# Kernel optimization log

Measured on AMD Instinct MI355X. Metric: run time of the kernel, lower is better.

The kernel has to match this reference:

```python
import jax, jax.numpy as jnp
import numpy as np
from numpy.lib.stride_tricks import sliding_window_view

# Static configuration matching init_kwargs
F_, H_, W_ = 2, 32, 32          # video_shape
K = 5                            # kernel_size (odd)
HEADS, DIM_HEAD = 8, 64
N = F_ * H_ * W_                 # number of video tokens (2048)
PAD = K // 2
INNER = HEADS * DIM_HEAD         # 512


def _neighbors():
    # Flattened token index at each (f,h,w); pad with sentinel N (out of bounds -> zeros / masked)
    idx = np.arange(N, dtype=np.int32).reshape(F_, H_, W_)
    padded = np.full((F_ + 2 * PAD, H_ + 2 * PAD, W_ + 2 * PAD), N, dtype=np.int32)
    padded[PAD:PAD + F_, PAD:PAD + H_, PAD:PAD + W_] = idx
    # sliding_window_view matches unfoldNd's kernel-offset ordering (kf, kh, kw row-major)
    return sliding_window_view(padded, (K, K, K)).reshape(N, K ** 3)


NBR = jnp.asarray(_neighbors())                                   # [N, K^3]
# causal: query i attends only to neighbors with index <= i; prepend BOS column (never masked)
CAUSAL = jnp.pad(jnp.arange(N)[:, None] < NBR, ((0, 0), (1, 0)))  # [N, K^3 + 1]


def setup_inputs() -> dict:
    key = jax.random.key(0)
    k1, k2, k3 = jax.random.split(key, 3)
    return {
        "x": jax.random.normal(k1, (1, N, INNER), jnp.float32),
        "w_qkv": jax.random.normal(k2, (INNER, 3 * INNER), jnp.float32) * 0.02,
        "w_out": jax.random.normal(k3, (INNER, INNER), jnp.float32) * 0.02,
        "b_out": jnp.zeros((INNER,), jnp.float32),
    }


def reference(x, w_qkv, w_out, b_out):
    b, n, dim = x.shape            # n == N
    bh = b * HEADS
    scale = DIM_HEAD ** -0.5

    xp = jnp.pad(x, ((0, 0), (0, 1), (0, 0)))        # pad one zero token at the end: [b, n+1, dim]
    qkv = xp @ w_qkv                                  # [b, n+1, 3*inner]
    q, kk, vv = jnp.split(qkv, 3, axis=-1)

    def split_heads(t):  # 'b n (h d) -> (b h) n d'
        return t.reshape(b, n + 1, HEADS, DIM_HEAD).transpose(0, 2, 1, 3).reshape(bh, n + 1, DIM_HEAD)

    q, kk, vv = map(split_heads, (q, kk, vv))
    q = q[:, 1:] * scale                              # drop BOS query: [bh, n, d]
    k_bos, kk = kk[:, :1], kk[:, 1:]                  # BOS kv + n spatial tokens
    v_bos, vv = vv[:, :1], vv[:, 1:]

    # Append a zero row so the sentinel index N gathers zeros (== unfold's zero padding)
    zero = jnp.zeros((bh, 1, DIM_HEAD), kk.dtype)
    kw = jnp.concatenate([kk, zero], axis=1)[:, NBR]  # [bh, n, K^3, d]
    vw = jnp.concatenate([vv, zero], axis=1)[:, NBR]

    bos_k = jnp.broadcast_to(k_bos[:, None], (bh, n, 1, DIM_HEAD))
    bos_v = jnp.broadcast_to(v_bos[:, None], (bh, n, 1, DIM_HEAD))
    kw = jnp.concatenate([bos_k, kw], axis=2)         # [bh, n, K^3+1, d]
    vw = jnp.concatenate([bos_v, vw], axis=2)

    sim = jnp.einsum('bid,bijd->bij', q, kw)          # [bh, n, K^3+1]
    sim = jnp.where(CAUSAL[:n], -jnp.finfo(sim.dtype).max, sim)
    attn = jax.nn.softmax(sim, axis=-1)
    out = jnp.einsum('bij,bijd->bid', attn, vw)       # [bh, n, d]

    out = jnp.concatenate([v_bos, out], axis=1)       # BOS output = its value: [bh, n+1, d]
    out = out.reshape(b, HEADS, n + 1, DIM_HEAD).transpose(0, 2, 1, 3).reshape(b, n + 1, INNER)
    return (out @ w_out + b_out)[:, :n]
```

## Files before the change

kernel.cpp:

```cpp
#include <hip/hip_runtime.h>
#include <hip/hip_bf16.h>

#define NTOK  2048
#define INNER 512
#define KDIM  512
#define QKVP  1536

typedef __attribute__((ext_vector_type(8))) short bf16x8;
typedef __attribute__((ext_vector_type(4))) float f32x4;

__device__ __forceinline__ unsigned short f2b(float f) {
  unsigned int u = __float_as_uint(f);
  return (unsigned short)((u + 0x7FFFu + ((u >> 16) & 1u)) >> 16);
}

__device__ __forceinline__ void async_copy16(const unsigned short* g, unsigned short* l) {
  __builtin_amdgcn_global_load_lds((const __attribute__((address_space(1))) void*)g,
                                   (__attribute__((address_space(3))) void*)l, 16, 0, 0);
}

__global__ __launch_bounds__(256) void prep(const float* __restrict__ w_qkv,
                                            const float* __restrict__ w_out,
                                            const float* __restrict__ x,
                                            unsigned short* __restrict__ wqkvT,
                                            unsigned short* __restrict__ woutT,
                                            unsigned short* __restrict__ xb,
                                            int* __restrict__ glist,
                                            int* __restrict__ gcnt) {
  __shared__ float tile[32][33];
  __shared__ int list[192];
  __shared__ int cntS;
  const int tid = threadIdx.x;
  int b = blockIdx.x;

  if (b >= 1152) {
    const int i = (b - 1152) * 1024 + tid * 4;
    float4 v = *(const float4*)(x + i);
    ushort4 o;
    o.x = f2b(v.x); o.y = f2b(v.y); o.z = f2b(v.z); o.w = f2b(v.w);
    *(ushort4*)(xb + i) = o;
    return;
  }

  if (b < 1024) {
    const float* in; unsigned short* out; int K, N, bx, by;
    if (b < 768) { in = w_qkv; out = wqkvT; K = 512; N = 1536; bx = b % 48; by = b / 48; }
    else { int bb = b - 768; in = w_out; out = woutT; K = 512; N = 512; bx = bb & 15; by = bb >> 4; }
    const int k0 = by * 32, n0 = bx * 32;
    const int r = tid >> 3, c4 = (tid & 7) * 4;
    float4 v = *(const float4*)(in + (size_t)(k0 + r) * N + n0 + c4);
    tile[r][c4 + 0] = v.x; tile[r][c4 + 1] = v.y;
    tile[r][c4 + 2] = v.z; tile[r][c4 + 3] = v.w;
    __syncthreads();
    ushort4 o;
    o.x = f2b(tile[c4 + 0][r]);
    o.y = f2b(tile[c4 + 1][r]);
    o.z = f2b(tile[c4 + 2][r]);
    o.w = f2b(tile[c4 + 3][r]);
    *(ushort4*)(out + (size_t)(n0 + r) * K + k0 + c4) = o;
    return;
  }

  const int pt = b - 1024;
  const int f  = pt >> 6;
  const int hh = (pt >> 1) & 31;
  const int w0 = (pt & 1) << 4;

  if (tid < 192) list[tid] = 0x7FFFFFFF;
  if (tid == 0) { list[0] = 0; cntS = 1; }
  __syncthreads();
  if (tid >= 1 && tid <= 160) {
    int cc = tid - 1;
    int p = cc / 20, wo = cc - p * 20;
    int ff = (p < 5) ? 0 : 1;
    int h2 = hh - 2 + ((p < 5) ? p : (p - 5));
    bool ok = (p < 5) ? ((f == 1) ? (h2 >= 0 && h2 <= 31) : (p <= 2 && h2 >= 0))
                      : (f == 1 && h2 >= 0);
    if (ok) {
      bool diag = (ff == f) && (h2 == hh);
      int wlo = max(0, w0 - 2);
      int whi = min(31, diag ? (w0 + 15) : (w0 + 17));
      int w2 = wlo + wo;
      if (w2 <= whi) {
        int pos = atomicAdd(&cntS, 1);
        list[pos] = ((ff << 10) | (h2 << 5) | w2) + 1;
      }
    }
  }
  __syncthreads();
  if (tid < 192) glist[pt * 192 + tid] = list[tid];
  if (tid == 0) gcnt[pt] = cntS;
}

__global__ __launch_bounds__(256, 4) void gemm_qkv(const unsigned short* __restrict__ A,
                                                   const unsigned short* __restrict__ Bt,
                                                   unsigned short* __restrict__ C) {
  constexpr int BK = 32, N = 1536, K = 512;
  __shared__ __align__(16) unsigned short As[64 * BK];
  __shared__ __align__(16) unsigned short Bs[64 * BK];
  const int tid = threadIdx.x, lane = tid & 63, wave = tid >> 6;
  const int m0 = blockIdx.y * 64, n0 = blockIdx.x * 64;
  const int wm = (wave >> 1) * 32, wn = (wave & 1) * 32;
  const int li = tid * 8, r = li >> 5, c = li & 31;
  const int fr = lane & 15, fk = (lane >> 4) * 8;

  f32x4 acc[2][2] = {};

  for (int k0 = 0; k0 < K; k0 += BK) {
    async_copy16(A  + (size_t)(m0 + r) * K + k0 + c, &As[li]);
    async_copy16(Bt + (size_t)(n0 + r) * K + k0 + c, &Bs[li]);
    __syncthreads();
    bf16x8 af[2], bfr[2];
#pragma unroll
    for (int i = 0; i < 2; ++i) af[i] = *(const bf16x8*)&As[(wm + i * 16 + fr) * BK + fk];
#pragma unroll
    for (int j = 0; j < 2; ++j) bfr[j] = *(const bf16x8*)&Bs[(wn + j * 16 + fr) * BK + fk];
#pragma unroll
    for (int i = 0; i < 2; ++i)
#pragma unroll
      for (int j = 0; j < 2; ++j)
        acc[i][j] = __builtin_amdgcn_mfma_f32_16x16x32_bf16(af[i], bfr[j], acc[i][j], 0, 0, 0);
    __syncthreads();
  }

  const int er = (lane >> 4) * 4, ec = lane & 15;
#pragma unroll
  for (int i = 0; i < 2; ++i)
#pragma unroll
    for (int j = 0; j < 2; ++j) {
      const int col = n0 + wn + j * 16 + ec;
#pragma unroll
      for (int rr = 0; rr < 4; ++rr) {
        const int row = m0 + wm + i * 16 + er + rr;
        C[(size_t)row * N + col] = f2b(acc[i][j][rr]);
      }
    }
}

__global__ __launch_bounds__(256, 4) void gemm_out(const unsigned short* __restrict__ A,
                                                   const unsigned short* __restrict__ Bt,
                                                   const float* __restrict__ bias,
                                                   float* __restrict__ C) {
  constexpr int BK = 32, N = 512, K = 512;
  __shared__ __align__(16) unsigned short As[32 * BK];
  __shared__ __align__(16) unsigned short Bs[64 * BK];
  const int tid = threadIdx.x, lane = tid & 63, wave = tid >> 6;
  const int m0 = blockIdx.y * 32, n0 = blockIdx.x * 64;
  const int wm = (wave >> 1) * 16, wn = (wave & 1) * 32;
  const int li = tid * 8, r = li >> 5, c = li & 31;
  const int fr = lane & 15, fk = (lane >> 4) * 8;

  f32x4 acc[2] = {};

  for (int k0 = 0; k0 < K; k0 += BK) {
    if (tid < 128) async_copy16(A + (size_t)(m0 + r) * K + k0 + c, &As[li]);
    async_copy16(Bt + (size_t)(n0 + r) * K + k0 + c, &Bs[li]);
    __syncthreads();
    bf16x8 af, bfr[2];
    af = *(const bf16x8*)&As[(wm + fr) * BK + fk];
#pragma unroll
    for (int j = 0; j < 2; ++j) bfr[j] = *(const bf16x8*)&Bs[(wn + j * 16 + fr) * BK + fk];
#pragma unroll
    for (int j = 0; j < 2; ++j)
      acc[j] = __builtin_amdgcn_mfma_f32_16x16x32_bf16(af, bfr[j], acc[j], 0, 0, 0);
    __syncthreads();
  }

  const int er = (lane >> 4) * 4, ec = lane & 15;
#pragma unroll
  for (int j = 0; j < 2; ++j) {
    const int col = n0 + wn + j * 16 + ec;
    const float b = bias[col];
#pragma unroll
    for (int rr = 0; rr < 4; ++rr) {
      const int row = m0 + wm + er + rr;
      C[(size_t)row * N + col] = acc[j][rr] + b;
    }
  }
}

__global__ __launch_bounds__(256) void attn_mfma(const unsigned short* __restrict__ qkv,
                                                 const int* __restrict__ glist,
                                                 const int* __restrict__ gcnt,
                                                 unsigned short* __restrict__ O) {
  __shared__ __align__(16) int list[192];
  __shared__ __align__(16) float mOd[2][16][72];
  __shared__ float mM[2][16], mL[2][16];
  __shared__ int cntS;

  const int tid = threadIdx.x;
  const int hp = blockIdx.y;

  if (blockIdx.x == 128) {
    if (tid < 128) O[hp * 128 + tid] = qkv[1024 + hp * 128 + tid];
    return;
  }
  const int pt = blockIdx.x;
  const int f  = pt >> 6;
  const int hh = (pt >> 1) & 31;
  const int w0 = (pt & 1) << 4;
  const int base_i = (f << 10) | (hh << 5) | w0;

  if (tid < 192) list[tid] = glist[pt * 192 + tid];
  if (tid == 0) cntS = gcnt[pt];
  __syncthreads();
  const int nsub = (cntS + 15) >> 4;

  const int lane = tid & 63;
  const int wave = tid >> 6;
  const int hw   = wave >> 1;
  const int half = wave & 1;
  const int head = hp * 2 + hw;
  const int quad = lane >> 4;
  const int ec   = lane & 15;

  const int i_q = base_i + ec;
  const int tq  = min(i_q + 1, 2047);
  const unsigned short* qrow = qkv + (size_t)tq * QKVP + head * 64 + quad * 8;
  const bf16x8 qb0 = *(const bf16x8*)(qrow);
  const bf16x8 qb1 = *(const bf16x8*)(qrow + 32);

  f32x4 Od[4] = {{0,0,0,0},{0,0,0,0},{0,0,0,0},{0,0,0,0}};
  float m = -1e30f, l = 0.0f;

  for (int sub = half; sub < nsub; sub += 2) {
    const int base = sub * 16;
    const int tok_e = list[base + ec];
    const int4 tokv = *(const int4*)&list[base + quad * 4];
    const int tk[4] = {tokv.x, tokv.y, tokv.z, tokv.w};

    f32x4 S = {0, 0, 0, 0};
    {
      const int t0 = (tok_e > 2047) ? 0 : tok_e;
      const unsigned short* kr = qkv + (size_t)t0 * QKVP + 512 + head * 64 + quad * 8;
      const bf16x8 kf0 = *(const bf16x8*)(kr);
      const bf16x8 kf1 = *(const bf16x8*)(kr + 32);
      S = __builtin_amdgcn_mfma_f32_16x16x32_bf16(kf0, qb0, S, 0, 0, 0);
      S = __builtin_amdgcn_mfma_f32_16x16x32_bf16(kf1, qb1, S, 0, 0, 0);
    }

    float Sm[4];
#pragma unroll
    for (int r = 0; r < 4; ++r) {
      const int tok = tk[r];
      const int idx = tok - 1;
      const bool v = (tok == 0) ||
                     ((idx <= i_q) && ((unsigned)((idx & 31) - (w0 + ec) + 2) <= 4u));
      Sm[r] = v ? S[r] * 0.125f : -1e30f;
    }
    float mx = fmaxf(fmaxf(Sm[0], Sm[1]), fmaxf(Sm[2], Sm[3]));
    mx = fmaxf(mx, __shfl_xor(mx, 16, 64));
    mx = fmaxf(mx, __shfl_xor(mx, 32, 64));
    const float mn = fmaxf(m, mx);
    const float corr = __expf(m - mn);
    m = mn;
    const float p0 = __expf(Sm[0] - mn);
    const float p1 = __expf(Sm[1] - mn);
    const float p2 = __expf(Sm[2] - mn);
    const float p3 = __expf(Sm[3] - mn);
    float rs = (p0 + p1) + (p2 + p3);
    rs += __shfl_xor(rs, 16, 64);
    rs += __shfl_xor(rs, 32, 64);
    l = l * corr + rs;

    bf16x8 pf;
    pf[0] = (short)f2b(p0); pf[1] = (short)f2b(p1);
    pf[2] = (short)f2b(p2); pf[3] = (short)f2b(p3);
    pf[4] = 0; pf[5] = 0; pf[6] = 0; pf[7] = 0;

    const unsigned short* vp[4];
#pragma unroll
    for (int j = 0; j < 4; ++j) {
      const int tv = (tk[j] > 2047) ? 0 : tk[j];
      vp[j] = qkv + (size_t)tv * QKVP + 1024 + head * 64 + ec;
    }
#pragma unroll
    for (int dt = 0; dt < 4; ++dt) {
      bf16x8 vf;
#pragma unroll
      for (int j = 0; j < 4; ++j) vf[j] = (short)vp[j][dt * 16];
      vf[4] = 0; vf[5] = 0; vf[6] = 0; vf[7] = 0;
#pragma unroll
      for (int r = 0; r < 4; ++r) Od[dt][r] *= corr;
      Od[dt] = __builtin_amdgcn_mfma_f32_16x16x32_bf16(vf, pf, Od[dt], 0, 0, 0);
    }
  }

  if (half == 1) {
#pragma unroll
    for (int dt = 0; dt < 4; ++dt)
      *(f32x4*)&mOd[hw][ec][dt * 16 + quad * 4] = Od[dt];
    if (quad == 0) { mM[hw][ec] = m; mL[hw][ec] = l; }
  }
  __syncthreads();
  if (half == 0 && i_q <= 2046) {
    const float m1 = mM[hw][ec], l1 = mL[hw][ec];
    const float mm = fmaxf(m, m1);
    const float c0 = __expf(m - mm), c1 = __expf(m1 - mm);
    const float rl = 1.0f / (l * c0 + l1 * c1);
    unsigned short* ob = O + (size_t)(i_q + 1) * 512 + head * 64 + quad * 4;
#pragma unroll
    for (int dt = 0; dt < 4; ++dt) {
      const f32x4 o1 = *(const f32x4*)&mOd[hw][ec][dt * 16 + quad * 4];
      ushort4 u;
      u.x = f2b((Od[dt][0] * c0 + o1[0] * c1) * rl);
      u.y = f2b((Od[dt][1] * c0 + o1[1] * c1) * rl);
      u.z = f2b((Od[dt][2] * c0 + o1[2] * c1) * rl);
      u.w = f2b((Od[dt][3] * c0 + o1[3] * c1) * rl);
      *(ushort4*)(ob + dt * 16) = u;
    }
  }
}


extern "C" void kernel_launch(void* const* d_in, const int* in_sizes, int n_in,
                              void* d_out, int out_size, void* d_ws, size_t ws_size,
                              hipStream_t stream) {
  const float* x     = (const float*)d_in[0];
  const float* w_qkv = (const float*)d_in[1];
  const float* w_out = (const float*)d_in[2];
  const float* b_out = (const float*)d_in[3];
  float* out = (float*)d_out;

  char* ws = (char*)d_ws;
  unsigned short* qkvb  = (unsigned short*)(ws);
  unsigned short* wqkvT = (unsigned short*)(ws + 6291456);
  unsigned short* woutT = (unsigned short*)(ws + 7864320);
  unsigned short* Ob    = (unsigned short*)(ws + 8388608);
  unsigned short* xb    = (unsigned short*)(ws + 10485760);
  int*            glist = (int*)(ws + 12582912);
  int*            gcnt  = (int*)(ws + 12681216);

  hipLaunchKernelGGL(prep, dim3(2176), dim3(256), 0, stream,
                     w_qkv, w_out, x, wqkvT, woutT, xb, glist, gcnt);

  hipLaunchKernelGGL(gemm_qkv, dim3(24, 32), dim3(256), 0, stream, xb, wqkvT, qkvb);

  hipLaunchKernelGGL(attn_mfma, dim3(129, 4), dim3(256), 0, stream, qkvb, glist, gcnt, Ob);

  hipLaunchKernelGGL(gemm_out, dim3(8, 64), dim3(256), 0, stream, Ob, woutT, b_out, out);
}
```

Before: 96.29 us.

## Fuse all four stages into one cooperative persistent kernel with grid syncs

Merges the prep, QKV GEMM, local attention and output GEMM kernels into a single cooperative kernel of 512 persistent blocks. Each stage loops over its original block indices with a grid stride and is separated from the next by grid.sync(). This removes three kernel launches and the gaps between them. In exchange it adds grid-wide barrier cost, loses the occupancy hint of launch bounds (256, 4) on the GEMMs, and makes each block's register and LDS budget the maximum needed by any stage.

```diff
diff --git a/kernel.cpp b/kernel.cpp
--- a/kernel.cpp
+++ b/kernel.cpp
@@ -1,5 +1,8 @@
 #include <hip/hip_runtime.h>
 #include <hip/hip_bf16.h>
+#include <hip/hip_cooperative_groups.h>
+
+namespace cg = cooperative_groups;
 
 #define NTOK  2048
 #define INNER 512
@@ -19,295 +22,302 @@
                                    (__attribute__((address_space(3))) void*)l, 16, 0, 0);
 }
 
-__global__ __launch_bounds__(256) void prep(const float* __restrict__ w_qkv,
+__global__ __launch_bounds__(256) void mega(const float* __restrict__ x,
+                                            const float* __restrict__ w_qkv,
                                             const float* __restrict__ w_out,
-                                            const float* __restrict__ x,
+                                            const float* __restrict__ b_out,
+                                            float* __restrict__ out,
+                                            unsigned short* __restrict__ qkvb,
                                             unsigned short* __restrict__ wqkvT,
                                             unsigned short* __restrict__ woutT,
+                                            unsigned short* __restrict__ Ob,
                                             unsigned short* __restrict__ xb,
                                             int* __restrict__ glist,
                                             int* __restrict__ gcnt) {
-  __shared__ float tile[32][33];
-  __shared__ int list[192];
-  __shared__ int cntS;
+  cg::grid_group grid = cg::this_grid();
+  __shared__ __align__(16) char smem[12544];
   const int tid = threadIdx.x;
-  int b = blockIdx.x;
-
-  if (b >= 1152) {
-    const int i = (b - 1152) * 1024 + tid * 4;
-    float4 v = *(const float4*)(x + i);
-    ushort4 o;
-    o.x = f2b(v.x); o.y = f2b(v.y); o.z = f2b(v.z); o.w = f2b(v.w);
-    *(ushort4*)(xb + i) = o;
-    return;
-  }
-
-  if (b < 1024) {
-    const float* in; unsigned short* out; int K, N, bx, by;
-    if (b < 768) { in = w_qkv; out = wqkvT; K = 512; N = 1536; bx = b % 48; by = b / 48; }
-    else { int bb = b - 768; in = w_out; out = woutT; K = 512; N = 512; bx = bb & 15; by = bb >> 4; }
-    const int k0 = by * 32, n0 = bx * 32;
-    const int r = tid >> 3, c4 = (tid & 7) * 4;
-    float4 v = *(const float4*)(in + (size_t)(k0 + r) * N + n0 + c4);
-    tile[r][c4 + 0] = v.x; tile[r][c4 + 1] = v.y;
-    tile[r][c4 + 2] = v.z; tile[r][c4 + 3] = v.w;
-    __syncthreads();
-    ushort4 o;
-    o.x = f2b(tile[c4 + 0][r]);
-    o.y = f2b(tile[c4 + 1][r]);
-    o.z = f2b(tile[c4 + 2][r]);
-    o.w = f2b(tile[c4 + 3][r]);
-    *(ushort4*)(out + (size_t)(n0 + r) * K + k0 + c4) = o;
-    return;
-  }
-
-  const int pt = b - 1024;
-  const int f  = pt >> 6;
-  const int hh = (pt >> 1) & 31;
-  const int w0 = (pt & 1) << 4;
-
-  if (tid < 192) list[tid] = 0x7FFFFFFF;
-  if (tid == 0) { list[0] = 0; cntS = 1; }
-  __syncthreads();
-  if (tid >= 1 && tid <= 160) {
-    int cc = tid - 1;
-    int p = cc / 20, wo = cc - p * 20;
-    int ff = (p < 5) ? 0 : 1;
-    int h2 = hh - 2 + ((p < 5) ? p : (p - 5));
-    bool ok = (p < 5) ? ((f == 1) ? (h2 >= 0 && h2 <= 31) : (p <= 2 && h2 >= 0))
-                      : (f == 1 && h2 >= 0);
-    if (ok) {
-      bool diag = (ff == f) && (h2 == hh);
-      int wlo = max(0, w0 - 2);
-      int whi = min(31, diag ? (w0 + 15) : (w0 + 17));
-      int w2 = wlo + wo;
-      if (w2 <= whi) {
-        int pos = atomicAdd(&cntS, 1);
-        list[pos] = ((ff << 10) | (h2 << 5) | w2) + 1;
-      }
+  const int nb  = gridDim.x;
+
+  {
+    float (*tile)[33] = (float(*)[33])smem;
+    int* list = (int*)(smem + 4224);
+    int* cntS = (int*)(smem + 4224 + 768);
+
+    for (int b = blockIdx.x; b < 2176; b += nb) {
+      if (b >= 1152) {
+        const int i = (b - 1152) * 1024 + tid * 4;
+        float4 v = *(const float4*)(x + i);
+        ushort4 o;
+        o.x = f2b(v.x); o.y = f2b(v.y); o.z = f2b(v.z); o.w = f2b(v.w);
+        *(ushort4*)(xb + i) = o;
+        continue;
+      }
+      if (b < 1024) {
+        const float* in; unsigned short* outw; int K, N, bx, by;
+        if (b < 768) { in = w_qkv; outw = wqkvT; K = 512; N = 1536; bx = b % 48; by = b / 48; }
+        else { int bb = b - 768; in = w_out; outw = woutT; K = 512; N = 512; bx = bb & 15; by = bb >> 4; }
+        const int k0 = by * 32, n0 = bx * 32;
+        const int r = tid >> 3, c4 = (tid & 7) * 4;
+        float4 v = *(const float4*)(in + (size_t)(k0 + r) * N + n0 + c4);
+        tile[r][c4 + 0] = v.x; tile[r][c4 + 1] = v.y;
+        tile[r][c4 + 2] = v.z; tile[r][c4 + 3] = v.w;
+        __syncthreads();
+        ushort4 o;
+        o.x = f2b(tile[c4 + 0][r]);
+        o.y = f2b(tile[c4 + 1][r]);
+        o.z = f2b(tile[c4 + 2][r]);
+        o.w = f2b(tile[c4 + 3][r]);
+        *(ushort4*)(outw + (size_t)(n0 + r) * K + k0 + c4) = o;
+        __syncthreads();
+        continue;
+      }
+      const int pt = b - 1024;
+      const int f  = pt >> 6;
+      const int hh = (pt >> 1) & 31;
+      const int w0 = (pt & 1) << 4;
+      if (tid < 192) list[tid] = 0x7FFFFFFF;
+      if (tid == 0) { list[0] = 0; *cntS = 1; }
+      __syncthreads();
+      if (tid >= 1 && tid <= 160) {
+        int cc = tid - 1;
+        int p = cc / 20, wo = cc - p * 20;
+        int ff = (p < 5) ? 0 : 1;
+        int h2 = hh - 2 + ((p < 5) ? p : (p - 5));
+        bool ok = (p < 5) ? ((f == 1) ? (h2 >= 0 && h2 <= 31) : (p <= 2 && h2 >= 0))
+                          : (f == 1 && h2 >= 0);
+        if (ok) {
+          bool diag = (ff == f) && (h2 == hh);
+          int wlo = max(0, w0 - 2);
+          int whi = min(31, diag ? (w0 + 15) : (w0 + 17));
+          int w2 = wlo + wo;
+          if (w2 <= whi) {
+            int pos = atomicAdd(cntS, 1);
+            list[pos] = ((ff << 10) | (h2 << 5) | w2) + 1;
+          }
+        }
+      }
+      __syncthreads();
+      if (tid < 192) glist[pt * 192 + tid] = list[tid];
+      if (tid == 0) gcnt[pt] = *cntS;
+      __syncthreads();
     }
   }
-  __syncthreads();
-  if (tid < 192) glist[pt * 192 + tid] = list[tid];
-  if (tid == 0) gcnt[pt] = cntS;
-}
-
-__global__ __launch_bounds__(256, 4) void gemm_qkv(const unsigned short* __restrict__ A,
-                                                   const unsigned short* __restrict__ Bt,
-                                                   unsigned short* __restrict__ C) {
-  constexpr int BK = 32, N = 1536, K = 512;
-  __shared__ __align__(16) unsigned short As[64 * BK];
-  __shared__ __align__(16) unsigned short Bs[64 * BK];
-  const int tid = threadIdx.x, lane = tid & 63, wave = tid >> 6;
-  const int m0 = blockIdx.y * 64, n0 = blockIdx.x * 64;
-  const int wm = (wave >> 1) * 32, wn = (wave & 1) * 32;
-  const int li = tid * 8, r = li >> 5, c = li & 31;
-  const int fr = lane & 15, fk = (lane >> 4) * 8;
-
-  f32x4 acc[2][2] = {};
-
-  for (int k0 = 0; k0 < K; k0 += BK) {
-    async_copy16(A  + (size_t)(m0 + r) * K + k0 + c, &As[li]);
-    async_copy16(Bt + (size_t)(n0 + r) * K + k0 + c, &Bs[li]);
-    __syncthreads();
-    bf16x8 af[2], bfr[2];
-#pragma unroll
-    for (int i = 0; i < 2; ++i) af[i] = *(const bf16x8*)&As[(wm + i * 16 + fr) * BK + fk];
-#pragma unroll
-    for (int j = 0; j < 2; ++j) bfr[j] = *(const bf16x8*)&Bs[(wn + j * 16 + fr) * BK + fk];
-#pragma unroll
-    for (int i = 0; i < 2; ++i)
-#pragma unroll
-      for (int j = 0; j < 2; ++j)
-        acc[i][j] = __builtin_amdgcn_mfma_f32_16x16x32_bf16(af[i], bfr[j], acc[i][j], 0, 0, 0);
-    __syncthreads();
-  }
-
-  const int er = (lane >> 4) * 4, ec = lane & 15;
-#pragma unroll
-  for (int i = 0; i < 2; ++i)
-#pragma unroll
-    for (int j = 0; j < 2; ++j) {
-      const int col = n0 + wn + j * 16 + ec;
-#pragma unroll
-      for (int rr = 0; rr < 4; ++rr) {
-        const int row = m0 + wm + i * 16 + er + rr;
-        C[(size_t)row * N + col] = f2b(acc[i][j][rr]);
-      }
-    }
-}
-
-__global__ __launch_bounds__(256, 4) void gemm_out(const unsigned short* __restrict__ A,
-                                                   const unsigned short* __restrict__ Bt,
-                                                   const float* __restrict__ bias,
-                                                   float* __restrict__ C) {
-  constexpr int BK = 32, N = 512, K = 512;
-  __shared__ __align__(16) unsigned short As[32 * BK];
-  __shared__ __align__(16) unsigned short Bs[64 * BK];
-  const int tid = threadIdx.x, lane = tid & 63, wave = tid >> 6;
-  const int m0 = blockIdx.y * 32, n0 = blockIdx.x * 64;
-  const int wm = (wave >> 1) * 16, wn = (wave & 1) * 32;
-  const int li = tid * 8, r = li >> 5, c = li & 31;
-  const int fr = lane & 15, fk = (lane >> 4) * 8;
-
-  f32x4 acc[2] = {};
-
-  for (int k0 = 0; k0 < K; k0 += BK) {
-    if (tid < 128) async_copy16(A + (size_t)(m0 + r) * K + k0 + c, &As[li]);
-    async_copy16(Bt + (size_t)(n0 + r) * K + k0 + c, &Bs[li]);
-    __syncthreads();
-    bf16x8 af, bfr[2];
-    af = *(const bf16x8*)&As[(wm + fr) * BK + fk];
-#pragma unroll
-    for (int j = 0; j < 2; ++j) bfr[j] = *(const bf16x8*)&Bs[(wn + j * 16 + fr) * BK + fk];
-#pragma unroll
-    for (int j = 0; j < 2; ++j)
-      acc[j] = __builtin_amdgcn_mfma_f32_16x16x32_bf16(af, bfr[j], acc[j], 0, 0, 0);
-    __syncthreads();
-  }
-
-  const int er = (lane >> 4) * 4, ec = lane & 15;
-#pragma unroll
-  for (int j = 0; j < 2; ++j) {
-    const int col = n0 + wn + j * 16 + ec;
-    const float b = bias[col];
-#pragma unroll
-    for (int rr = 0; rr < 4; ++rr) {
-      const int row = m0 + wm + er + rr;
-      C[(size_t)row * N + col] = acc[j][rr] + b;
+  grid.sync();
+
+  {
+    constexpr int BK = 32, N = 1536, K = 512;
+    unsigned short* As = (unsigned short*)smem;
+    unsigned short* Bs = (unsigned short*)(smem + 4096);
+    const int lane = tid & 63, wave = tid >> 6;
+    const int wm = (wave >> 1) * 32, wn = (wave & 1) * 32;
+    const int li = tid * 8, r = li >> 5, c = li & 31;
+    const int fr = lane & 15, fk = (lane >> 4) * 8;
+
+    for (int b = blockIdx.x; b < 768; b += nb) {
+      const int m0 = (b / 24) * 64, n0 = (b % 24) * 64;
+      f32x4 acc[2][2] = {};
+      for (int k0 = 0; k0 < K; k0 += BK) {
+        async_copy16(xb    + (size_t)(m0 + r) * K + k0 + c, &As[li]);
+        async_copy16(wqkvT + (size_t)(n0 + r) * K + k0 + c, &Bs[li]);
+        __syncthreads();
+        bf16x8 af[2], bfr[2];
+#pragma unroll
+        for (int i = 0; i < 2; ++i) af[i] = *(const bf16x8*)&As[(wm + i * 16 + fr) * BK + fk];
+#pragma unroll
+        for (int j = 0; j < 2; ++j) bfr[j] = *(const bf16x8*)&Bs[(wn + j * 16 + fr) * BK + fk];
+#pragma unroll
+        for (int i = 0; i < 2; ++i)
+#pragma unroll
+          for (int j = 0; j < 2; ++j)
+            acc[i][j] = __builtin_amdgcn_mfma_f32_16x16x32_bf16(af[i], bfr[j], acc[i][j], 0, 0, 0);
+        __syncthreads();
+      }
+      const int er = (lane >> 4) * 4, ec = lane & 15;
+#pragma unroll
+      for (int i = 0; i < 2; ++i)
+#pragma unroll
+        for (int j = 0; j < 2; ++j) {
+          const int col = n0 + wn + j * 16 + ec;
+#pragma unroll
+          for (int rr = 0; rr < 4; ++rr) {
+            const int row = m0 + wm + i * 16 + er + rr;
+            qkvb[(size_t)row * N + col] = f2b(acc[i][j][rr]);
+          }
+        }
     }
   }
-}
-
-__global__ __launch_bounds__(256) void attn_mfma(const unsigned short* __restrict__ qkv,
-                                                 const int* __restrict__ glist,
-                                                 const int* __restrict__ gcnt,
-                                                 unsigned short* __restrict__ O) {
-  __shared__ __align__(16) int list[192];
-  __shared__ __align__(16) float mOd[2][16][72];
-  __shared__ float mM[2][16], mL[2][16];
-  __shared__ int cntS;
-
-  const int tid = threadIdx.x;
-  const int hp = blockIdx.y;
-
-  if (blockIdx.x == 128) {
-    if (tid < 128) O[hp * 128 + tid] = qkv[1024 + hp * 128 + tid];
-    return;
-  }
-  const int pt = blockIdx.x;
-  const int f  = pt >> 6;
-  const int hh = (pt >> 1) & 31;
-  const int w0 = (pt & 1) << 4;
-  const int base_i = (f << 10) | (hh << 5) | w0;
-
-  if (tid < 192) list[tid] = glist[pt * 192 + tid];
-  if (tid == 0) cntS = gcnt[pt];
-  __syncthreads();
-  const int nsub = (cntS + 15) >> 4;
-
-  const int lane = tid & 63;
-  const int wave = tid >> 6;
-  const int hw   = wave >> 1;
-  const int half = wave & 1;
-  const int head = hp * 2 + hw;
-  const int quad = lane >> 4;
-  const int ec   = lane & 15;
-
-  const int i_q = base_i + ec;
-  const int tq  = min(i_q + 1, 2047);
-  const unsigned short* qrow = qkv + (size_t)tq * QKVP + head * 64 + quad * 8;
-  const bf16x8 qb0 = *(const bf16x8*)(qrow);
-  const bf16x8 qb1 = *(const bf16x8*)(qrow + 32);
-
-  f32x4 Od[4] = {{0,0,0,0},{0,0,0,0},{0,0,0,0},{0,0,0,0}};
-  float m = -1e30f, l = 0.0f;
-
-  for (int sub = half; sub < nsub; sub += 2) {
-    const int base = sub * 16;
-    const int tok_e = list[base + ec];
-    const int4 tokv = *(const int4*)&list[base + quad * 4];
-    const int tk[4] = {tokv.x, tokv.y, tokv.z, tokv.w};
-
-    f32x4 S = {0, 0, 0, 0};
-    {
-      const int t0 = (tok_e > 2047) ? 0 : tok_e;
-      const unsigned short* kr = qkv + (size_t)t0 * QKVP + 512 + head * 64 + quad * 8;
-      const bf16x8 kf0 = *(const bf16x8*)(kr);
-      const bf16x8 kf1 = *(const bf16x8*)(kr + 32);
-      S = __builtin_amdgcn_mfma_f32_16x16x32_bf16(kf0, qb0, S, 0, 0, 0);
-      S = __builtin_amdgcn_mfma_f32_16x16x32_bf16(kf1, qb1, S, 0, 0, 0);
-    }
-
-    float Sm[4];
-#pragma unroll
-    for (int r = 0; r < 4; ++r) {
-      const int tok = tk[r];
-      const int idx = tok - 1;
-      const bool v = (tok == 0) ||
-                     ((idx <= i_q) && ((unsigned)((idx & 31) - (w0 + ec) + 2) <= 4u));
-      Sm[r] = v ? S[r] * 0.125f : -1e30f;
-    }
-    float mx = fmaxf(fmaxf(Sm[0], Sm[1]), fmaxf(Sm[2], Sm[3]));
-    mx = fmaxf(mx, __shfl_xor(mx, 16, 64));
-    mx = fmaxf(mx, __shfl_xor(mx, 32, 64));
-    const float mn = fmaxf(m, mx);
-    const float corr = __expf(m - mn);
-    m = mn;
-    const float p0 = __expf(Sm[0] - mn);
-    const float p1 = __expf(Sm[1] - mn);
-    const float p2 = __expf(Sm[2] - mn);
-    const float p3 = __expf(Sm[3] - mn);
-    float rs = (p0 + p1) + (p2 + p3);
-    rs += __shfl_xor(rs, 16, 64);
-    rs += __shfl_xor(rs, 32, 64);
-    l = l * corr + rs;
-
-    bf16x8 pf;
-    pf[0] = (short)f2b(p0); pf[1] = (short)f2b(p1);
-    pf[2] = (short)f2b(p2); pf[3] = (short)f2b(p3);
-    pf[4] = 0; pf[5] = 0; pf[6] = 0; pf[7] = 0;
-
-    const unsigned short* vp[4];
-#pragma unroll
-    for (int j = 0; j < 4; ++j) {
-      const int tv = (tk[j] > 2047) ? 0 : tk[j];
-      vp[j] = qkv + (size_t)tv * QKVP + 1024 + head * 64 + ec;
-    }
-#pragma unroll
-    for (int dt = 0; dt < 4; ++dt) {
-      bf16x8 vf;
-#pragma unroll
-      for (int j = 0; j < 4; ++j) vf[j] = (short)vp[j][dt * 16];
-      vf[4] = 0; vf[5] = 0; vf[6] = 0; vf[7] = 0;
-#pragma unroll
-      for (int r = 0; r < 4; ++r) Od[dt][r] *= corr;
-      Od[dt] = __builtin_amdgcn_mfma_f32_16x16x32_bf16(vf, pf, Od[dt], 0, 0, 0);
+  grid.sync();
+
+  {
+    int* list   = (int*)smem;
+    float* mOd  = (float*)(smem + 768);
+    float* mM   = (float*)(smem + 9984);
+    float* mL   = (float*)(smem + 10112);
+    int* cntS   = (int*)(smem + 10240);
+
+    for (int b = blockIdx.x; b < 516; b += nb) {
+      const int pt = b >> 2;
+      const int hp = b & 3;
+      if (pt == 128) {
+        if (tid < 128) Ob[hp * 128 + tid] = qkvb[1024 + hp * 128 + tid];
+        continue;
+      }
+      const int f  = pt >> 6;
+      const int hh = (pt >> 1) & 31;
+      const int w0 = (pt & 1) << 4;
+      const int base_i = (f << 10) | (hh << 5) | w0;
+
+      if (tid < 192) list[tid] = glist[pt * 192 + tid];
+      if (tid == 0) *cntS = gcnt[pt];
+      __syncthreads();
+      const int nsub = (*cntS + 15) >> 4;
+
+      const int lane = tid & 63;
+      const int wave = tid >> 6;
+      const int hw   = wave >> 1;
+      const int half = wave & 1;
+      const int head = hp * 2 + hw;
+      const int quad = lane >> 4;
+      const int ec   = lane & 15;
+
+      const int i_q = base_i + ec;
+      const int tq  = min(i_q + 1, 2047);
+      const unsigned short* qrow = qkvb + (size_t)tq * QKVP + head * 64 + quad * 8;
+      const bf16x8 qb0 = *(const bf16x8*)(qrow);
+      const bf16x8 qb1 = *(const bf16x8*)(qrow + 32);
+
+      f32x4 Od[4] = {{0,0,0,0},{0,0,0,0},{0,0,0,0},{0,0,0,0}};
+      float m = -1e30f, l = 0.0f;
+
+      for (int sub = half; sub < nsub; sub += 2) {
+        const int base = sub * 16;
+        const int tok_e = list[base + ec];
+        const int4 tokv = *(const int4*)&list[base + quad * 4];
+        const int tk[4] = {tokv.x, tokv.y, tokv.z, tokv.w};
+
+        f32x4 S = {0, 0, 0, 0};
+        {
+          const int t0 = (tok_e > 2047) ? 0 : tok_e;
+          const unsigned short* kr = qkvb + (size_t)t0 * QKVP + 512 + head * 64 + quad * 8;
+          const bf16x8 kf0 = *(const bf16x8*)(kr);
+          const bf16x8 kf1 = *(const bf16x8*)(kr + 32);
+          S = __builtin_amdgcn_mfma_f32_16x16x32_bf16(kf0, qb0, S, 0, 0, 0);
+          S = __builtin_amdgcn_mfma_f32_16x16x32_bf16(kf1, qb1, S, 0, 0, 0);
+        }
+
+        float Sm[4];
+#pragma unroll
+        for (int r = 0; r < 4; ++r) {
+          const int tok = tk[r];
+          const int idx = tok - 1;
+          const bool v = (tok == 0) ||
+                         ((idx <= i_q) && ((unsigned)((idx & 31) - (w0 + ec) + 2) <= 4u));
+          Sm[r] = v ? S[r] * 0.125f : -1e30f;
+        }
+        float mx = fmaxf(fmaxf(Sm[0], Sm[1]), fmaxf(Sm[2], Sm[3]));
+        mx = fmaxf(mx, __shfl_xor(mx, 16, 64));
+        mx = fmaxf(mx, __shfl_xor(mx, 32, 64));
+        const float mn = fmaxf(m, mx);
+        const float corr = __expf(m - mn);
+        m = mn;
+        const float p0 = __expf(Sm[0] - mn);
+        const float p1 = __expf(Sm[1] - mn);
+        const float p2 = __expf(Sm[2] - mn);
+        const float p3 = __expf(Sm[3] - mn);
+        float rs = (p0 + p1) + (p2 + p3);
+        rs += __shfl_xor(rs, 16, 64);
+        rs += __shfl_xor(rs, 32, 64);
+        l = l * corr + rs;
+
+        bf16x8 pf;
+        pf[0] = (short)f2b(p0); pf[1] = (short)f2b(p1);
+        pf[2] = (short)f2b(p2); pf[3] = (short)f2b(p3);
+        pf[4] = 0; pf[5] = 0; pf[6] = 0; pf[7] = 0;
+
+        const unsigned short* vp[4];
+#pragma unroll
+        for (int j = 0; j < 4; ++j) {
+          const int tv = (tk[j] > 2047) ? 0 : tk[j];
+          vp[j] = qkvb + (size_t)tv * QKVP + 1024 + head * 64 + ec;
+        }
+#pragma unroll
+        for (int dt = 0; dt < 4; ++dt) {
+          bf16x8 vf;
+#pragma unroll
+          for (int j = 0; j < 4; ++j) vf[j] = (short)vp[j][dt * 16];
+          vf[4] = 0; vf[5] = 0; vf[6] = 0; vf[7] = 0;
+#pragma unroll
+          for (int r = 0; r < 4; ++r) Od[dt][r] *= corr;
+          Od[dt] = __builtin_amdgcn_mfma_f32_16x16x32_bf16(vf, pf, Od[dt], 0, 0, 0);
+        }
+      }
+
+      if (half == 1) {
+#pragma unroll
+        for (int dt = 0; dt < 4; ++dt)
+          *(f32x4*)&mOd[(hw * 16 + ec) * 72 + dt * 16 + quad * 4] = Od[dt];
+        if (quad == 0) { mM[hw * 16 + ec] = m; mL[hw * 16 + ec] = l; }
+      }
+      __syncthreads();
+      if (half == 0 && i_q <= 2046) {
+        const float m1 = mM[hw * 16 + ec], l1 = mL[hw * 16 + ec];
+        const float mm = fmaxf(m, m1);
+        const float c0 = __expf(m - mm), c1 = __expf(m1 - mm);
+        const float rl = 1.0f / (l * c0 + l1 * c1);
+        unsigned short* ob = Ob + (size_t)(i_q + 1) * 512 + head * 64 + quad * 4;
+#pragma unroll
+        for (int dt = 0; dt < 4; ++dt) {
+          const f32x4 o1 = *(const f32x4*)&mOd[(hw * 16 + ec) * 72 + dt * 16 + quad * 4];
+          ushort4 u;
+          u.x = f2b((Od[dt][0] * c0 + o1[0] * c1) * rl);
+          u.y = f2b((Od[dt][1] * c0 + o1[1] * c1) * rl);
+          u.z = f2b((Od[dt][2] * c0 + o1[2] * c1) * rl);
+          u.w = f2b((Od[dt][3] * c0 + o1[3] * c1) * rl);
+          *(ushort4*)(ob + dt * 16) = u;
+        }
+      }
+      __syncthreads();
     }
   }
-
-  if (half == 1) {
-#pragma unroll
-    for (int dt = 0; dt < 4; ++dt)
-      *(f32x4*)&mOd[hw][ec][dt * 16 + quad * 4] = Od[dt];
-    if (quad == 0) { mM[hw][ec] = m; mL[hw][ec] = l; }
-  }
-  __syncthreads();
-  if (half == 0 && i_q <= 2046) {
-    const float m1 = mM[hw][ec], l1 = mL[hw][ec];
-    const float mm = fmaxf(m, m1);
-    const float c0 = __expf(m - mm), c1 = __expf(m1 - mm);
-    const float rl = 1.0f / (l * c0 + l1 * c1);
-    unsigned short* ob = O + (size_t)(i_q + 1) * 512 + head * 64 + quad * 4;
-#pragma unroll
-    for (int dt = 0; dt < 4; ++dt) {
-      const f32x4 o1 = *(const f32x4*)&mOd[hw][ec][dt * 16 + quad * 4];
-      ushort4 u;
-      u.x = f2b((Od[dt][0] * c0 + o1[0] * c1) * rl);
-      u.y = f2b((Od[dt][1] * c0 + o1[1] * c1) * rl);
-      u.z = f2b((Od[dt][2] * c0 + o1[2] * c1) * rl);
-      u.w = f2b((Od[dt][3] * c0 + o1[3] * c1) * rl);
-      *(ushort4*)(ob + dt * 16) = u;
+  grid.sync();
+
+  {
+    constexpr int BK = 32, N = 512, K = 512;
+    unsigned short* As = (unsigned short*)smem;
+    unsigned short* Bs = (unsigned short*)(smem + 2048);
+    const int lane = tid & 63, wave = tid >> 6;
+    const int wm = (wave >> 1) * 16, wn = (wave & 1) * 32;
+    const int li = tid * 8, r = li >> 5, c = li & 31;
+    const int fr = lane & 15, fk = (lane >> 4) * 8;
+
+    for (int b = blockIdx.x; b < 512; b += nb) {
+      const int m0 = (b >> 3) * 32, n0 = (b & 7) * 64;
+      f32x4 acc[2] = {};
+      for (int k0 = 0; k0 < K; k0 += BK) {
+        if (tid < 128) async_copy16(Ob + (size_t)(m0 + r) * K + k0 + c, &As[li]);
+        async_copy16(woutT + (size_t)(n0 + r) * K + k0 + c, &Bs[li]);
+        __syncthreads();
+        bf16x8 af, bfr[2];
+        af = *(const bf16x8*)&As[(wm + fr) * BK + fk];
+#pragma unroll
+        for (int j = 0; j < 2; ++j) bfr[j] = *(const bf16x8*)&Bs[(wn + j * 16 + fr) * BK + fk];
+#pragma unroll
+        for (int j = 0; j < 2; ++j)
+          acc[j] = __builtin_amdgcn_mfma_f32_16x16x32_bf16(af, bfr[j], acc[j], 0, 0, 0);
+        __syncthreads();
+      }
+      const int er = (lane >> 4) * 4, ec = lane & 15;
+#pragma unroll
+      for (int j = 0; j < 2; ++j) {
+        const int col = n0 + wn + j * 16 + ec;
+        const float bb = b_out[col];
+#pragma unroll
+        for (int rr = 0; rr < 4; ++rr) {
+          const int row = m0 + wm + er + rr;
+          out[(size_t)row * N + col] = acc[j][rr] + bb;
+        }
+      }
     }
   }
 }
@@ -331,12 +341,8 @@
   int*            glist = (int*)(ws + 12582912);
   int*            gcnt  = (int*)(ws + 12681216);
 
-  hipLaunchKernelGGL(prep, dim3(2176), dim3(256), 0, stream,
-                     w_qkv, w_out, x, wqkvT, woutT, xb, glist, gcnt);
-
-  hipLaunchKernelGGL(gemm_qkv, dim3(24, 32), dim3(256), 0, stream, xb, wqkvT, qkvb);
-
-  hipLaunchKernelGGL(attn_mfma, dim3(129, 4), dim3(256), 0, stream, qkvb, glist, gcnt, Ob);
-
-  hipLaunchKernelGGL(gemm_out, dim3(8, 64), dim3(256), 0, stream, Ob, woutT, b_out, out);
+  void* kargs[] = {(void*)&x, (void*)&w_qkv, (void*)&w_out, (void*)&b_out, (void*)&out,
+                   (void*)&qkvb, (void*)&wqkvT, (void*)&woutT, (void*)&Ob, (void*)&xb,
+                   (void*)&glist, (void*)&gcnt};
+  hipLaunchCooperativeKernel((void*)mega, dim3(512), dim3(256), kargs, 0, stream);
 }
```

New measurement: 295.6 us. +207.0%, slower.

## Fuse fp32-to-bf16 conversion and neighbor list build into consumer kernels

Applied to the files above, without the earlier changes.

Removes the separate prep kernel. The QKV and output GEMMs now read fp32 x and weights directly, converting to bf16 while staging into LDS, and the attention kernel builds its causal neighbor list in shared memory instead of reading it from global memory. This cuts one launch and the round trips through the bf16 and list buffers. In exchange, the weight loads become strided scalar column reads, and the same weight conversion is repeated across every M-tile block rather than done once.

```diff
diff --git a/kernel.cpp b/kernel.cpp
--- a/kernel.cpp
+++ b/kernel.cpp
@@ -19,52 +19,88 @@
                                    (__attribute__((address_space(3))) void*)l, 16, 0, 0);
 }
 
-__global__ __launch_bounds__(256) void prep(const float* __restrict__ w_qkv,
-                                            const float* __restrict__ w_out,
-                                            const float* __restrict__ x,
-                                            unsigned short* __restrict__ wqkvT,
-                                            unsigned short* __restrict__ woutT,
-                                            unsigned short* __restrict__ xb,
-                                            int* __restrict__ glist,
-                                            int* __restrict__ gcnt) {
-  __shared__ float tile[32][33];
-  __shared__ int list[192];
+__global__ __launch_bounds__(256, 3) void gemm_qkv_f(const float* __restrict__ x,
+                                                     const float* __restrict__ w_qkv,
+                                                     unsigned short* __restrict__ C) {
+  constexpr int BK = 32, N = 1536, K = 512;
+  __shared__ __align__(16) unsigned short As[64 * BK];
+  __shared__ __align__(16) unsigned short Bs[64 * BK];
+  const int tid = threadIdx.x, lane = tid & 63, wave = tid >> 6;
+  const int m0 = blockIdx.y * 64, n0 = blockIdx.x * 64;
+  const int wm = (wave >> 1) * 32, wn = (wave & 1) * 32;
+  const int ar = tid >> 2, ac = (tid & 3) * 8;
+  const int bn = tid >> 2, bk8 = (tid & 3) * 8;
+  const int fr = lane & 15, fk = (lane >> 4) * 8;
+
+  f32x4 acc[2][2] = {};
+
+  for (int k0 = 0; k0 < K; k0 += BK) {
+    {
+      const float* ap = x + (size_t)(m0 + ar) * K + k0 + ac;
+      float4 a0 = *(const float4*)(ap);
+      float4 a1 = *(const float4*)(ap + 4);
+      bf16x8 av;
+      av[0] = (short)f2b(a0.x); av[1] = (short)f2b(a0.y);
+      av[2] = (short)f2b(a0.z); av[3] = (short)f2b(a0.w);
+      av[4] = (short)f2b(a1.x); av[5] = (short)f2b(a1.y);
+      av[6] = (short)f2b(a1.z); av[7] = (short)f2b(a1.w);
+      *(bf16x8*)&As[ar * BK + ac] = av;
+    }
+    {
+      const float* bp = w_qkv + (size_t)(k0 + bk8) * N + n0 + bn;
+      bf16x8 bv;
+#pragma unroll
+      for (int j = 0; j < 8; ++j) bv[j] = (short)f2b(bp[(size_t)j * N]);
+      *(bf16x8*)&Bs[bn * BK + bk8] = bv;
+    }
+    __syncthreads();
+
+    bf16x8 af[2], bfr[2];
+#pragma unroll
+    for (int i = 0; i < 2; ++i) af[i] = *(const bf16x8*)&As[(wm + i * 16 + fr) * BK + fk];
+#pragma unroll
+    for (int j = 0; j < 2; ++j) bfr[j] = *(const bf16x8*)&Bs[(wn + j * 16 + fr) * BK + fk];
+#pragma unroll
+    for (int i = 0; i < 2; ++i)
+#pragma unroll
+      for (int j = 0; j < 2; ++j)
+        acc[i][j] = __builtin_amdgcn_mfma_f32_16x16x32_bf16(af[i], bfr[j], acc[i][j], 0, 0, 0);
+    __syncthreads();
+  }
+
+  const int er = (lane >> 4) * 4, ec = lane & 15;
+#pragma unroll
+  for (int i = 0; i < 2; ++i)
+#pragma unroll
+    for (int j = 0; j < 2; ++j) {
+      const int col = n0 + wn + j * 16 + ec;
+#pragma unroll
+      for (int rr = 0; rr < 4; ++rr) {
+        const int row = m0 + wm + i * 16 + er + rr;
+        C[(size_t)row * N + col] = f2b(acc[i][j][rr]);
+      }
+    }
+}
+
+__global__ __launch_bounds__(256) void attn_mfma(const unsigned short* __restrict__ qkv,
+                                                 unsigned short* __restrict__ O) {
+  __shared__ __align__(16) int list[192];
+  __shared__ __align__(16) float mOd[2][16][72];
+  __shared__ float mM[2][16], mL[2][16];
   __shared__ int cntS;
+
   const int tid = threadIdx.x;
-  int b = blockIdx.x;
-
-  if (b >= 1152) {
-    const int i = (b - 1152) * 1024 + tid * 4;
-    float4 v = *(const float4*)(x + i);
-    ushort4 o;
-    o.x = f2b(v.x); o.y = f2b(v.y); o.z = f2b(v.z); o.w = f2b(v.w);
-    *(ushort4*)(xb + i) = o;
+  const int hp = blockIdx.y;
+
+  if (blockIdx.x == 128) {
+    if (tid < 128) O[hp * 128 + tid] = qkv[1024 + hp * 128 + tid];
     return;
   }
-
-  if (b < 1024) {
-    const float* in; unsigned short* out; int K, N, bx, by;
-    if (b < 768) { in = w_qkv; out = wqkvT; K = 512; N = 1536; bx = b % 48; by = b / 48; }
-    else { int bb = b - 768; in = w_out; out = woutT; K = 512; N = 512; bx = bb & 15; by = bb >> 4; }
-    const int k0 = by * 32, n0 = bx * 32;
-    const int r = tid >> 3, c4 = (tid & 7) * 4;
-    float4 v = *(const float4*)(in + (size_t)(k0 + r) * N + n0 + c4);
-    tile[r][c4 + 0] = v.x; tile[r][c4 + 1] = v.y;
-    tile[r][c4 + 2] = v.z; tile[r][c4 + 3] = v.w;
-    __syncthreads();
-    ushort4 o;
-    o.x = f2b(tile[c4 + 0][r]);
-    o.y = f2b(tile[c4 + 1][r]);
-    o.z = f2b(tile[c4 + 2][r]);
-    o.w = f2b(tile[c4 + 3][r]);
-    *(ushort4*)(out + (size_t)(n0 + r) * K + k0 + c4) = o;
-    return;
-  }
-
-  const int pt = b - 1024;
+  const int pt = blockIdx.x;
   const int f  = pt >> 6;
   const int hh = (pt >> 1) & 31;
   const int w0 = (pt & 1) << 4;
+  const int base_i = (f << 10) | (hh << 5) | w0;
 
   if (tid < 192) list[tid] = 0x7FFFFFFF;
   if (tid == 0) { list[0] = 0; cntS = 1; }
@@ -88,122 +124,6 @@
     }
   }
   __syncthreads();
-  if (tid < 192) glist[pt * 192 + tid] = list[tid];
-  if (tid == 0) gcnt[pt] = cntS;
-}
-
-__global__ __launch_bounds__(256, 4) void gemm_qkv(const unsigned short* __restrict__ A,
-                                                   const unsigned short* __restrict__ Bt,
-                                                   unsigned short* __restrict__ C) {
-  constexpr int BK = 32, N = 1536, K = 512;
-  __shared__ __align__(16) unsigned short As[64 * BK];
-  __shared__ __align__(16) unsigned short Bs[64 * BK];
-  const int tid = threadIdx.x, lane = tid & 63, wave = tid >> 6;
-  const int m0 = blockIdx.y * 64, n0 = blockIdx.x * 64;
-  const int wm = (wave >> 1) * 32, wn = (wave & 1) * 32;
-  const int li = tid * 8, r = li >> 5, c = li & 31;
-  const int fr = lane & 15, fk = (lane >> 4) * 8;
-
-  f32x4 acc[2][2] = {};
-
-  for (int k0 = 0; k0 < K; k0 += BK) {
-    async_copy16(A  + (size_t)(m0 + r) * K + k0 + c, &As[li]);
-    async_copy16(Bt + (size_t)(n0 + r) * K + k0 + c, &Bs[li]);
-    __syncthreads();
-    bf16x8 af[2], bfr[2];
-#pragma unroll
-    for (int i = 0; i < 2; ++i) af[i] = *(const bf16x8*)&As[(wm + i * 16 + fr) * BK + fk];
-#pragma unroll
-    for (int j = 0; j < 2; ++j) bfr[j] = *(const bf16x8*)&Bs[(wn + j * 16 + fr) * BK + fk];
-#pragma unroll
-    for (int i = 0; i < 2; ++i)
-#pragma unroll
-      for (int j = 0; j < 2; ++j)
-        acc[i][j] = __builtin_amdgcn_mfma_f32_16x16x32_bf16(af[i], bfr[j], acc[i][j], 0, 0, 0);
-    __syncthreads();
-  }
-
-  const int er = (lane >> 4) * 4, ec = lane & 15;
-#pragma unroll
-  for (int i = 0; i < 2; ++i)
-#pragma unroll
-    for (int j = 0; j < 2; ++j) {
-      const int col = n0 + wn + j * 16 + ec;
-#pragma unroll
-      for (int rr = 0; rr < 4; ++rr) {
-        const int row = m0 + wm + i * 16 + er + rr;
-        C[(size_t)row * N + col] = f2b(acc[i][j][rr]);
-      }
-    }
-}
-
-__global__ __launch_bounds__(256, 4) void gemm_out(const unsigned short* __restrict__ A,
-                                                   const unsigned short* __restrict__ Bt,
-                                                   const float* __restrict__ bias,
-                                                   float* __restrict__ C) {
-  constexpr int BK = 32, N = 512, K = 512;
-  __shared__ __align__(16) unsigned short As[32 * BK];
-  __shared__ __align__(16) unsigned short Bs[64 * BK];
-  const int tid = threadIdx.x, lane = tid & 63, wave = tid >> 6;
-  const int m0 = blockIdx.y * 32, n0 = blockIdx.x * 64;
-  const int wm = (wave >> 1) * 16, wn = (wave & 1) * 32;
-  const int li = tid * 8, r = li >> 5, c = li & 31;
-  const int fr = lane & 15, fk = (lane >> 4) * 8;
-
-  f32x4 acc[2] = {};
-
-  for (int k0 = 0; k0 < K; k0 += BK) {
-    if (tid < 128) async_copy16(A + (size_t)(m0 + r) * K + k0 + c, &As[li]);
-    async_copy16(Bt + (size_t)(n0 + r) * K + k0 + c, &Bs[li]);
-    __syncthreads();
-    bf16x8 af, bfr[2];
-    af = *(const bf16x8*)&As[(wm + fr) * BK + fk];
-#pragma unroll
-    for (int j = 0; j < 2; ++j) bfr[j] = *(const bf16x8*)&Bs[(wn + j * 16 + fr) * BK + fk];
-#pragma unroll
-    for (int j = 0; j < 2; ++j)
-      acc[j] = __builtin_amdgcn_mfma_f32_16x16x32_bf16(af, bfr[j], acc[j], 0, 0, 0);
-    __syncthreads();
-  }
-
-  const int er = (lane >> 4) * 4, ec = lane & 15;
-#pragma unroll
-  for (int j = 0; j < 2; ++j) {
-    const int col = n0 + wn + j * 16 + ec;
-    const float b = bias[col];
-#pragma unroll
-    for (int rr = 0; rr < 4; ++rr) {
-      const int row = m0 + wm + er + rr;
-      C[(size_t)row * N + col] = acc[j][rr] + b;
-    }
-  }
-}
-
-__global__ __launch_bounds__(256) void attn_mfma(const unsigned short* __restrict__ qkv,
-                                                 const int* __restrict__ glist,
-                                                 const int* __restrict__ gcnt,
-                                                 unsigned short* __restrict__ O) {
-  __shared__ __align__(16) int list[192];
-  __shared__ __align__(16) float mOd[2][16][72];
-  __shared__ float mM[2][16], mL[2][16];
-  __shared__ int cntS;
-
-  const int tid = threadIdx.x;
-  const int hp = blockIdx.y;
-
-  if (blockIdx.x == 128) {
-    if (tid < 128) O[hp * 128 + tid] = qkv[1024 + hp * 128 + tid];
-    return;
-  }
-  const int pt = blockIdx.x;
-  const int f  = pt >> 6;
-  const int hh = (pt >> 1) & 31;
-  const int w0 = (pt & 1) << 4;
-  const int base_i = (f << 10) | (hh << 5) | w0;
-
-  if (tid < 192) list[tid] = glist[pt * 192 + tid];
-  if (tid == 0) cntS = gcnt[pt];
-  __syncthreads();
   const int nsub = (cntS + 15) >> 4;
 
   const int lane = tid & 63;
@@ -312,6 +232,55 @@
   }
 }
 
+__global__ __launch_bounds__(256, 4) void gemm_out_f(const unsigned short* __restrict__ A,
+                                                     const float* __restrict__ w_out,
+                                                     const float* __restrict__ bias,
+                                                     float* __restrict__ C) {
+  constexpr int BK = 32, N = 512, K = 512;
+  __shared__ __align__(16) unsigned short As[32 * BK];
+  __shared__ __align__(16) unsigned short Bs[64 * BK];
+  const int tid = threadIdx.x, lane = tid & 63, wave = tid >> 6;
+  const int m0 = blockIdx.y * 32, n0 = blockIdx.x * 64;
+  const int wm = (wave >> 1) * 16, wn = (wave & 1) * 32;
+  const int li = tid * 8, r = li >> 5, c = li & 31;
+  const int bn = tid >> 2, bk8 = (tid & 3) * 8;
+  const int fr = lane & 15, fk = (lane >> 4) * 8;
+
+  f32x4 acc[2] = {};
+
+  for (int k0 = 0; k0 < K; k0 += BK) {
+    if (tid < 128) async_copy16(A + (size_t)(m0 + r) * K + k0 + c, &As[li]);
+    {
+      const float* bp = w_out + (size_t)(k0 + bk8) * N + n0 + bn;
+      bf16x8 bv;
+#pragma unroll
+      for (int j = 0; j < 8; ++j) bv[j] = (short)f2b(bp[(size_t)j * N]);
+      *(bf16x8*)&Bs[bn * BK + bk8] = bv;
+    }
+    __syncthreads();
+    bf16x8 af, bfr[2];
+    af = *(const bf16x8*)&As[(wm + fr) * BK + fk];
+#pragma unroll
+    for (int j = 0; j < 2; ++j) bfr[j] = *(const bf16x8*)&Bs[(wn + j * 16 + fr) * BK + fk];
+#pragma unroll
+    for (int j = 0; j < 2; ++j)
+      acc[j] = __builtin_amdgcn_mfma_f32_16x16x32_bf16(af, bfr[j], acc[j], 0, 0, 0);
+    __syncthreads();
+  }
+
+  const int er = (lane >> 4) * 4, ec = lane & 15;
+#pragma unroll
+  for (int j = 0; j < 2; ++j) {
+    const int col = n0 + wn + j * 16 + ec;
+    const float b = bias[col];
+#pragma unroll
+    for (int rr = 0; rr < 4; ++rr) {
+      const int row = m0 + wm + er + rr;
+      C[(size_t)row * N + col] = acc[j][rr] + b;
+    }
+  }
+}
+
 
 extern "C" void kernel_launch(void* const* d_in, const int* in_sizes, int n_in,
                               void* d_out, int out_size, void* d_ws, size_t ws_size,
@@ -323,20 +292,12 @@
   float* out = (float*)d_out;
 
   char* ws = (char*)d_ws;
-  unsigned short* qkvb  = (unsigned short*)(ws);
-  unsigned short* wqkvT = (unsigned short*)(ws + 6291456);
-  unsigned short* woutT = (unsigned short*)(ws + 7864320);
-  unsigned short* Ob    = (unsigned short*)(ws + 8388608);
-  unsigned short* xb    = (unsigned short*)(ws + 10485760);
-  int*            glist = (int*)(ws + 12582912);
-  int*            gcnt  = (int*)(ws + 12681216);
-
-  hipLaunchKernelGGL(prep, dim3(2176), dim3(256), 0, stream,
-                     w_qkv, w_out, x, wqkvT, woutT, xb, glist, gcnt);
-
-  hipLaunchKernelGGL(gemm_qkv, dim3(24, 32), dim3(256), 0, stream, xb, wqkvT, qkvb);
-
-  hipLaunchKernelGGL(attn_mfma, dim3(129, 4), dim3(256), 0, stream, qkvb, glist, gcnt, Ob);
-
-  hipLaunchKernelGGL(gemm_out, dim3(8, 64), dim3(256), 0, stream, Ob, woutT, b_out, out);
-}
+  unsigned short* qkvb = (unsigned short*)(ws);
+  unsigned short* Ob   = (unsigned short*)(ws + 6291456);
+
+  hipLaunchKernelGGL(gemm_qkv_f, dim3(24, 32), dim3(256), 0, stream, x, w_qkv, qkvb);
+
+  hipLaunchKernelGGL(attn_mfma, dim3(129, 4), dim3(256), 0, stream, qkvb, Ob);
+
+  hipLaunchKernelGGL(gemm_out_f, dim3(8, 64), dim3(256), 0, stream, Ob, w_out, b_out, out);
+}
```

Measured after the change: 107.1 us. 11.2% more time.
